# Kernel optimization log

Hardware: AMD Instinct MI355X
Metric: run time of the kernel (lower is better)

The kernel has to match this reference:

```python
import jax, jax.numpy as jnp
import numpy as np

B, D, H = 4096, 256, 1024
TRACE_STEPS = 10
T_FINAL = 1.0


def setup_inputs() -> dict:
    key = jax.random.key(0)
    k0, k1, k2 = jax.random.split(key, 3)
    s1 = 1.0 / np.sqrt(D + 1)
    s2 = 1.0 / np.sqrt(H)
    return {
        "x": jax.random.normal(k0, (B, D), dtype=jnp.float32),
        "W1": jax.random.uniform(k1, (D + 1, H), jnp.float32, -s1, s1),
        "b1": jnp.zeros((H,), jnp.float32),
        "W2": jax.random.uniform(k2, (H, D), jnp.float32, -s2, s2),
        "b2": jnp.zeros((D,), jnp.float32),
    }


def _odefun(params, t, z):
    # FFJORD vector field: tanh MLP on [z, t]. z: [B, D] -> [B, D]
    W1, b1, W2, b2 = params
    tcol = jnp.full((z.shape[0], 1), t, dtype=z.dtype)
    h = jnp.tanh(jnp.concatenate([z, tcol], axis=-1) @ W1 + b1)
    return h @ W2 + b2


def _rademacher(key, shape, dtype):
    # randint(0,2)*2-1, matching the torch probe construction
    return jax.random.randint(key, shape, 0, 2).astype(dtype) * 2.0 - 1.0


def _aug_dynamics(params, t, state, e):
    # state: [B, D+1] = [z | logp]; e: [TRACE_STEPS, B, D] Rademacher probes.
    # torch computes etf = grad((f*e).sum(), z) = e^T J, div = (e^T J)*e summed.
    # e^T J e == e . (J e), so forward-mode jvp gives identical math.
    z = state[:, :-1]
    f = lambda zz: _odefun(params, t, zz)

    def probe(ei):
        f_z, Je = jax.jvp(f, (z,), (ei,))
        return f_z, jnp.sum(Je * ei, axis=-1)  # [B]

    f_z, divs = jax.vmap(probe)(e)
    f_z = f_z[0]                       # primal identical across probes
    div_est = jnp.mean(divs, axis=0)   # average of trace_steps estimates
    return jnp.concatenate([f_z, -div_est[:, None]], axis=-1)


def reference(x, W1, b1, W2, b2):
    params = (W1, b1, W2, b2)
    Bx = x.shape[0]
    ekey = jax.random.key(42)
    probes = lambda i: _rademacher(jax.random.fold_in(ekey, i), (TRACE_STEPS, Bx, D), x.dtype)

    # initial augmented state: [z, logp=0]
    y0 = jnp.concatenate([x, jnp.zeros((Bx, 1), x.dtype)], axis=-1)

    # t_grid = [0, T] with 2 points -> fixed-grid rk4 takes ONE RK4 step of size T
    h = T_FINAL
    g = lambda t, y, i: _aug_dynamics(params, t, y, probes(i))
    k1 = g(0.0, y0, 0)
    k2 = g(0.5 * h, y0 + 0.5 * h * k1, 1)
    k3 = g(0.5 * h, y0 + 0.5 * h * k2, 2)
    k4 = g(h, y0 + h * k3, 3)
    y1 = y0 + (h / 6.0) * (k1 + 2.0 * k2 + 2.0 * k3 + k4)

    # module returns the full trajectory `output`: [len(t_grid), B, D+1]
    return jnp.stack([y0, y1], axis=0)
```

## Files before the change

kernel.cpp:

```cpp
#include <hip/hip_runtime.h>
#include <stdint.h>

#define BATCH 4096
#define DIMD  256
#define DIMH  1024
#define EPAD  264
#define NEPW  163840

typedef __attribute__((ext_vector_type(8))) short short8;
typedef __attribute__((ext_vector_type(4))) float float4v;

struct Keys4 { uint32_t a[4]; uint32_t b[4]; };

__host__ __device__ static inline uint32_t rotl32(uint32_t v, int r) {
#ifdef __HIP_DEVICE_COMPILE__
    return __builtin_amdgcn_alignbit(v, v, 32 - r);
#else
    return (v << r) | (v >> (32 - r));
#endif
}

__host__ __device__ static inline void tf2x32(uint32_t k0, uint32_t k1,
                                              uint32_t c0, uint32_t c1,
                                              uint32_t& o0, uint32_t& o1) {
    uint32_t ks0 = k0, ks1 = k1, ks2 = k0 ^ k1 ^ 0x1BD11BDAu;
    uint32_t x0 = c0 + ks0, x1 = c1 + ks1;
#define TF_R4(a, b, c, d)                                   \
    x0 += x1; x1 = rotl32(x1, a); x1 ^= x0;                 \
    x0 += x1; x1 = rotl32(x1, b); x1 ^= x0;                 \
    x0 += x1; x1 = rotl32(x1, c); x1 ^= x0;                 \
    x0 += x1; x1 = rotl32(x1, d); x1 ^= x0;
    TF_R4(13, 15, 26, 6)  x0 += ks1; x1 += ks2 + 1u;
    TF_R4(17, 29, 16, 24) x0 += ks2; x1 += ks0 + 2u;
    TF_R4(13, 15, 26, 6)  x0 += ks0; x1 += ks1 + 3u;
    TF_R4(17, 29, 16, 24) x0 += ks1; x1 += ks2 + 4u;
    TF_R4(13, 15, 26, 6)  x0 += ks2; x1 += ks0 + 5u;
#undef TF_R4
    o0 = x0; o1 = x1;
}

__device__ static inline short f2bf(float f) {
    uint32_t u = __float_as_uint(f);
    uint32_t r = (u + 0x7FFFu + ((u >> 16) & 1u)) >> 16;
    return (short)r;
}

__global__ __launch_bounds__(256) void k_prep(
    const float* __restrict__ x,  const float* __restrict__ W1,
    const float* __restrict__ W2, short* __restrict__ W1T,
    short* __restrict__ W2B, short* __restrict__ W2T,
    short* __restrict__ zb, float* __restrict__ dv,
    uint64_t* __restrict__ Ep0, uint32_t ek0, uint32_t ek1)
{
    const int idx = blockIdx.x * 256 + threadIdx.x;
    if (idx < 262144) {
        const int n = idx >> 8, d = idx & 255;
        W1T[idx] = f2bf(W1[d * DIMH + n]);
    } else if (idx < 524288) {
        const int i = idx - 262144;
        W2B[i] = f2bf(W2[i]);
    } else if (idx < 786432) {
        const int i = idx - 524288;
        const int d = i >> 10, k = i & 1023;
        W2T[i] = f2bf(W2[k * DIMD + d]);
    } else if (idx < 1835008) {
        const int i = idx - 786432;
        zb[i] = f2bf(x[i]);
    } else if (idx < 1851392) {
        dv[idx - 1835008] = 0.0f;
    } else {
        const uint32_t j = (uint32_t)(idx - 1851392);
        uint32_t y0, y1;
        tf2x32(ek0, ek1, 0u, j, y0, y1);
        uint64_t mask = __ballot(((y0 ^ y1) & 1u) != 0u);
        if ((threadIdx.x & 63) == 0)
            Ep0[j >> 6] = mask;
    }
}

__global__ __launch_bounds__(256) void k_pre_div(
    const short* __restrict__ Zb, const short* __restrict__ W1T,
    const short* __restrict__ W2B, const float* __restrict__ W1,
    const float* __restrict__ b1, float tval,
    const uint64_t* __restrict__ Ep, short* __restrict__ h_bf,
    float* __restrict__ divacc,
    uint64_t* __restrict__ EpNext, uint32_t nk0, uint32_t nk1, int do_egen)
{
    __shared__ short E[64 * EPAD];
    const int t = threadIdx.x;
    const int nt = blockIdx.x;
    const int b0 = blockIdx.y * 64;
    const int wave = t >> 6, lane = t & 63;
    const int col = lane & 15, kq = lane >> 4;
    const int n = nt * 64 + wave * 16 + col;

    short8 bufr[8];
#pragma unroll
    for (int ks = 0; ks < 8; ++ks)
        bufr[ks] = *(const short8*)&W1T[n * DIMD + ks * 32 + kq * 8];

    float sreg[4][4];
    const float add = tval * W1[DIMD * DIMH + n] + b1[n];
#pragma unroll
    for (int ms = 0; ms < 4; ++ms) {
        float4v acc = {0.f, 0.f, 0.f, 0.f};
#pragma unroll
        for (int ks = 0; ks < 8; ++ks) {
            short8 af = *(const short8*)&Zb[(b0 + ms * 16 + col) * DIMD + ks * 32 + kq * 8];
            acc = __builtin_amdgcn_mfma_f32_16x16x32_bf16(af, bufr[ks], acc, 0, 0, 0);
        }
#pragma unroll
        for (int r = 0; r < 4; ++r) {
            float hv = tanhf(acc[r] + add);
            h_bf[(b0 + ms * 16 + kq * 4 + r) * DIMH + n] = f2bf(hv);
            sreg[ms][r] = 1.0f - hv * hv;
        }
    }

    if (do_egen) {
        const uint32_t bflat = (uint32_t)(blockIdx.y * 16 + blockIdx.x);
        const uint32_t jbase = bflat * 10240u + (uint32_t)t;
#pragma unroll 2
        for (int w = 0; w < 40; ++w) {
            uint32_t j = jbase + (uint32_t)w * 256u;
            uint32_t y0, y1;
            tf2x32(nk0, nk1, 0u, j, y0, y1);
            uint64_t mask = __ballot(((y0 ^ y1) & 1u) != 0u);
            if (lane == 0)
                EpNext[j >> 6] = mask;
        }
    }

    short8 bvfr[8];
#pragma unroll
    for (int ks = 0; ks < 8; ++ks)
        bvfr[ks] = *(const short8*)&W2B[n * DIMD + ks * 32 + kq * 8];

    float rowacc[4][4];
#pragma unroll
    for (int a = 0; a < 4; ++a)
#pragma unroll
        for (int r = 0; r < 4; ++r) rowacc[a][r] = 0.0f;

    const int erow = t & 63, ecg = t >> 6;
    short* const edst = &E[erow * EPAD + ecg * 64];
    const uint64_t* const esrc = Ep + (size_t)b0 * 4 + erow * 4 + ecg;

#pragma unroll 1
    for (int probe = 0; probe < 10; ++probe) {
        __syncthreads();
        uint64_t w = esrc[(size_t)probe * BATCH * 4];
#pragma unroll
        for (int i = 0; i < 8; ++i) {
            short8 val;
#pragma unroll
            for (int k = 0; k < 8; ++k)
                val[k] = ((w >> (i * 8 + k)) & 1ull) ? (short)0x3F80 : (short)0xBF80u;
            *(short8*)&edst[i * 8] = val;
        }
        __syncthreads();

#pragma unroll
        for (int ms = 0; ms < 4; ++ms) {
            const short* arow = &E[(ms * 16 + col) * EPAD + kq * 8];
            float4v u = {0.f, 0.f, 0.f, 0.f}, v = {0.f, 0.f, 0.f, 0.f};
#pragma unroll
            for (int ks = 0; ks < 8; ++ks) {
                short8 af = *(const short8*)&arow[ks * 32];
                u = __builtin_amdgcn_mfma_f32_16x16x32_bf16(af, bufr[ks], u, 0, 0, 0);
                v = __builtin_amdgcn_mfma_f32_16x16x32_bf16(af, bvfr[ks], v, 0, 0, 0);
            }
#pragma unroll
            for (int r = 0; r < 4; ++r)
                rowacc[ms][r] += u[r] * sreg[ms][r] * v[r];
        }
    }

#pragma unroll
    for (int ms = 0; ms < 4; ++ms) {
#pragma unroll
        for (int r = 0; r < 4; ++r) {
            float p = rowacc[ms][r];
            p += __shfl_xor(p, 1, 64);
            p += __shfl_xor(p, 2, 64);
            p += __shfl_xor(p, 4, 64);
            p += __shfl_xor(p, 8, 64);
            rowacc[ms][r] = p;
        }
    }
    if (col == 0) {
#pragma unroll
        for (int ms = 0; ms < 4; ++ms)
#pragma unroll
            for (int r = 0; r < 4; ++r)
                atomicAdd(&divacc[b0 + ms * 16 + kq * 4 + r], rowacc[ms][r] * 0.1f);
    }
}

__global__ __launch_bounds__(256) void k_fz2(
    const short* __restrict__ Hb, const short* __restrict__ W2T,
    const float* __restrict__ b2, const float* __restrict__ x,
    float* __restrict__ fz, float cnext, int write_zb, short* __restrict__ zb)
{
    const int t = threadIdx.x;
    const int wave = t >> 6, lane = t & 63;
    const int col = lane & 15, kq = lane >> 4;
    const int m0 = blockIdx.x * 16;
    const int n0 = wave * 64;

    float4v acc[4];
#pragma unroll
    for (int ns = 0; ns < 4; ++ns) acc[ns] = (float4v){0.f, 0.f, 0.f, 0.f};

    const short* ap = &Hb[(m0 + col) * DIMH + kq * 8];
    short8 a_cur = *(const short8*)ap;
    short8 b_cur[4];
#pragma unroll
    for (int ns = 0; ns < 4; ++ns)
        b_cur[ns] = *(const short8*)&W2T[(n0 + ns * 16 + col) * DIMH + kq * 8];

    for (int ks = 0; ks < 31; ++ks) {
        short8 a_nxt = *(const short8*)&ap[(ks + 1) * 32];
        short8 b_nxt[4];
#pragma unroll
        for (int ns = 0; ns < 4; ++ns)
            b_nxt[ns] = *(const short8*)&W2T[(n0 + ns * 16 + col) * DIMH + (ks + 1) * 32 + kq * 8];
#pragma unroll
        for (int ns = 0; ns < 4; ++ns)
            acc[ns] = __builtin_amdgcn_mfma_f32_16x16x32_bf16(a_cur, b_cur[ns], acc[ns], 0, 0, 0);
        a_cur = a_nxt;
#pragma unroll
        for (int ns = 0; ns < 4; ++ns) b_cur[ns] = b_nxt[ns];
    }
#pragma unroll
    for (int ns = 0; ns < 4; ++ns)
        acc[ns] = __builtin_amdgcn_mfma_f32_16x16x32_bf16(a_cur, b_cur[ns], acc[ns], 0, 0, 0);

#pragma unroll
    for (int ns = 0; ns < 4; ++ns) {
        const int n = n0 + ns * 16 + col;
        const float bias = b2[n];
#pragma unroll
        for (int r = 0; r < 4; ++r) {
            const int m = m0 + kq * 4 + r;
            const float val = acc[ns][r] + bias;
            fz[m * DIMD + n] = val;
            if (write_zb)
                zb[m * DIMD + n] = f2bf(x[m * DIMD + n] + cnext * val);
        }
    }
}

__global__ __launch_bounds__(256) void k_out(
    const float* __restrict__ x, const float* __restrict__ fz,
    const float* __restrict__ divacc, float* __restrict__ out)
{
    const int idx = blockIdx.x * 256 + threadIdx.x;
    const int TOT = BATCH * (DIMD + 1);
    if (idx >= TOT) return;
    const int b = idx / (DIMD + 1);
    const int c = idx - b * (DIMD + 1);
    const float sixth = 1.0f / 6.0f;
    if (c < DIMD) {
        float xv = x[b * DIMD + c];
        int o = b * DIMD + c;
        float f1 = fz[o];
        float f2 = fz[BATCH * DIMD + o];
        float f3 = fz[2 * BATCH * DIMD + o];
        float f4 = fz[3 * BATCH * DIMD + o];
        out[idx] = xv;
        out[TOT + idx] = xv + (f1 + 2.0f * f2 + 2.0f * f3 + f4) * sixth;
    } else {
        float d1 = divacc[b];
        float d2 = divacc[BATCH + b];
        float d3 = divacc[2 * BATCH + b];
        float d4 = divacc[3 * BATCH + b];
        out[idx] = 0.0f;
        out[TOT + idx] = -(d1 + 2.0f * d2 + 2.0f * d3 + d4) * sixth;
    }
}

extern "C" void kernel_launch(void* const* d_in, const int* in_sizes, int n_in,
                              void* d_out, int out_size, void* d_ws, size_t ws_size,
                              hipStream_t stream) {
    const float* x  = (const float*)d_in[0];
    const float* W1 = (const float*)d_in[1];
    const float* b1 = (const float*)d_in[2];
    const float* W2 = (const float*)d_in[3];
    const float* b2 = (const float*)d_in[4];
    float* out = (float*)d_out;

    char* ws = (char*)d_ws;
    short* hb    = (short*)(ws);
    float* fz    = (float*)(ws + 8388608);
    short* zb    = (short*)(ws + 25165824);
    short* w1t   = (short*)(ws + 27262976);
    short* w2b   = (short*)(ws + 27787264);
    short* w2t   = (short*)(ws + 28311552);
    float* dv    = (float*)(ws + 28835840);
    uint64_t* ep = (uint64_t*)(ws + 28901376);

    Keys4 keys;
    for (uint32_t i = 0; i < 4; ++i) {
        uint32_t f0, f1, g0, g1;
        tf2x32(0u, 42u, 0u, i, f0, f1);
        tf2x32(f0, f1, 0u, 1u, g0, g1);
        keys.a[i] = g0;
        keys.b[i] = g1;
    }

    k_prep<<<48192, 256, 0, stream>>>(x, W1, W2, w1t, w2b, w2t, zb, dv,
                                      ep, keys.a[0], keys.b[0]);

    const float tvals[4] = {0.0f, 0.5f, 0.5f, 1.0f};
    const float cnext[4] = {0.5f, 0.5f, 1.0f, 0.0f};
    for (int s = 0; s < 4; ++s) {
        const int last = (s == 3);
        k_pre_div<<<dim3(16, 64), 256, 0, stream>>>(
            zb, w1t, w2b, W1, b1, tvals[s], ep + (size_t)s * NEPW,
            hb, dv + (size_t)s * BATCH,
            ep + (size_t)(s + 1) * NEPW,
            last ? 0u : keys.a[s + 1], last ? 0u : keys.b[s + 1],
            last ? 0 : 1);
        k_fz2<<<256, 256, 0, stream>>>(hb, w2t, b2, x,
                                       fz + (size_t)s * BATCH * DIMD,
                                       cnext[s], (s < 3) ? 1 : 0, zb);
    }
    int tot = BATCH * (DIMD + 1);
    k_out<<<(tot + 255) / 256, 256, 0, stream>>>(x, fz, dv, out);
}
```

Baseline: 531.9 us.

## Store probes as expanded bf16 in global memory, drop LDS staging, accumulate RK sum

Probe vectors are now written to global memory as full bf16 ±1 values (double-buffered across stages) instead of packed bitmasks. The MFMA A-operands are then read directly from global memory, which removes the LDS expansion step and the two barriers per probe. Generation of the next stage's probes is interleaved inside the probe loop. The per-stage f outputs are folded into a single running RK4 weighted sum, which shrinks the workspace and the final kernel's reads. In exchange, probe traffic grows roughly 16x (about 20 MB per stage, written and read), and uncoalesced global A-loads replace LDS reads.

Result: slower. 1.055 ms (+98.4%).

```diff
diff --git a/kernel.cpp b/kernel.cpp
--- a/kernel.cpp
+++ b/kernel.cpp
@@ -4,8 +4,7 @@
 #define BATCH 4096
 #define DIMD  256
 #define DIMH  1024
-#define EPAD  264
-#define NEPW  163840
+#define NEEL  10485760
 
 typedef __attribute__((ext_vector_type(8))) short short8;
 typedef __attribute__((ext_vector_type(4))) float float4v;
@@ -50,7 +49,7 @@
     const float* __restrict__ W2, short* __restrict__ W1T,
     short* __restrict__ W2B, short* __restrict__ W2T,
     short* __restrict__ zb, float* __restrict__ dv,
-    uint64_t* __restrict__ Ep0, uint32_t ek0, uint32_t ek1)
+    short* __restrict__ E0, uint32_t ek0, uint32_t ek1)
 {
     const int idx = blockIdx.x * 256 + threadIdx.x;
     if (idx < 262144) {
@@ -72,9 +71,7 @@
         const uint32_t j = (uint32_t)(idx - 1851392);
         uint32_t y0, y1;
         tf2x32(ek0, ek1, 0u, j, y0, y1);
-        uint64_t mask = __ballot(((y0 ^ y1) & 1u) != 0u);
-        if ((threadIdx.x & 63) == 0)
-            Ep0[j >> 6] = mask;
+        E0[j] = ((y0 ^ y1) & 1u) ? (short)0x3F80 : (short)0xBF80u;
     }
 }
 
@@ -82,11 +79,10 @@
     const short* __restrict__ Zb, const short* __restrict__ W1T,
     const short* __restrict__ W2B, const float* __restrict__ W1,
     const float* __restrict__ b1, float tval,
-    const uint64_t* __restrict__ Ep, short* __restrict__ h_bf,
+    const short* __restrict__ Ecur, short* __restrict__ h_bf,
     float* __restrict__ divacc,
-    uint64_t* __restrict__ EpNext, uint32_t nk0, uint32_t nk1, int do_egen)
+    short* __restrict__ Enext, uint32_t nk0, uint32_t nk1, int do_egen)
 {
-    __shared__ short E[64 * EPAD];
     const int t = threadIdx.x;
     const int nt = blockIdx.x;
     const int b0 = blockIdx.y * 64;
@@ -94,10 +90,12 @@
     const int col = lane & 15, kq = lane >> 4;
     const int n = nt * 64 + wave * 16 + col;
 
-    short8 bufr[8];
-#pragma unroll
-    for (int ks = 0; ks < 8; ++ks)
+    short8 bufr[8], bvfr[8];
+#pragma unroll
+    for (int ks = 0; ks < 8; ++ks) {
         bufr[ks] = *(const short8*)&W1T[n * DIMD + ks * 32 + kq * 8];
+        bvfr[ks] = *(const short8*)&W2B[n * DIMD + ks * 32 + kq * 8];
+    }
 
     float sreg[4][4];
     const float add = tval * W1[DIMD * DIMH + n] + b1[n];
@@ -117,52 +115,27 @@
         }
     }
 
-    if (do_egen) {
-        const uint32_t bflat = (uint32_t)(blockIdx.y * 16 + blockIdx.x);
-        const uint32_t jbase = bflat * 10240u + (uint32_t)t;
-#pragma unroll 2
-        for (int w = 0; w < 40; ++w) {
-            uint32_t j = jbase + (uint32_t)w * 256u;
-            uint32_t y0, y1;
-            tf2x32(nk0, nk1, 0u, j, y0, y1);
-            uint64_t mask = __ballot(((y0 ^ y1) & 1u) != 0u);
-            if (lane == 0)
-                EpNext[j >> 6] = mask;
-        }
-    }
-
-    short8 bvfr[8];
-#pragma unroll
-    for (int ks = 0; ks < 8; ++ks)
-        bvfr[ks] = *(const short8*)&W2B[n * DIMD + ks * 32 + kq * 8];
-
     float rowacc[4][4];
 #pragma unroll
     for (int a = 0; a < 4; ++a)
 #pragma unroll
         for (int r = 0; r < 4; ++r) rowacc[a][r] = 0.0f;
 
-    const int erow = t & 63, ecg = t >> 6;
-    short* const edst = &E[erow * EPAD + ecg * 64];
-    const uint64_t* const esrc = Ep + (size_t)b0 * 4 + erow * 4 + ecg;
+    const uint32_t bflat = (uint32_t)(blockIdx.y * 16 + blockIdx.x);
+    const uint32_t jbase = bflat * 10240u + (uint32_t)t;
 
 #pragma unroll 1
     for (int probe = 0; probe < 10; ++probe) {
-        __syncthreads();
-        uint64_t w = esrc[(size_t)probe * BATCH * 4];
-#pragma unroll
-        for (int i = 0; i < 8; ++i) {
-            short8 val;
-#pragma unroll
-            for (int k = 0; k < 8; ++k)
-                val[k] = ((w >> (i * 8 + k)) & 1ull) ? (short)0x3F80 : (short)0xBF80u;
-            *(short8*)&edst[i * 8] = val;
-        }
-        __syncthreads();
-
+        const short* Ep = Ecur + (size_t)probe * (BATCH * DIMD) + (size_t)b0 * DIMD;
 #pragma unroll
         for (int ms = 0; ms < 4; ++ms) {
-            const short* arow = &E[(ms * 16 + col) * EPAD + kq * 8];
+            if (do_egen) {
+                uint32_t j = jbase + (uint32_t)(probe * 4 + ms) * 256u;
+                uint32_t y0, y1;
+                tf2x32(nk0, nk1, 0u, j, y0, y1);
+                Enext[j] = ((y0 ^ y1) & 1u) ? (short)0x3F80 : (short)0xBF80u;
+            }
+            const short* arow = Ep + (ms * 16 + col) * DIMD + kq * 8;
             float4v u = {0.f, 0.f, 0.f, 0.f}, v = {0.f, 0.f, 0.f, 0.f};
 #pragma unroll
             for (int ks = 0; ks < 8; ++ks) {
@@ -200,7 +173,8 @@
 __global__ __launch_bounds__(256) void k_fz2(
     const short* __restrict__ Hb, const short* __restrict__ W2T,
     const float* __restrict__ b2, const float* __restrict__ x,
-    float* __restrict__ fz, float cnext, int write_zb, short* __restrict__ zb)
+    float* __restrict__ rksum, float cw, int first,
+    float cnext, int write_zb, short* __restrict__ zb)
 {
     const int t = threadIdx.x;
     const int wave = t >> 6, lane = t & 63;
@@ -243,16 +217,18 @@
 #pragma unroll
         for (int r = 0; r < 4; ++r) {
             const int m = m0 + kq * 4 + r;
+            const int o = m * DIMD + n;
             const float val = acc[ns][r] + bias;
-            fz[m * DIMD + n] = val;
+            const float contrib = cw * val;
+            rksum[o] = first ? contrib : (rksum[o] + contrib);
             if (write_zb)
-                zb[m * DIMD + n] = f2bf(x[m * DIMD + n] + cnext * val);
+                zb[o] = f2bf(x[o] + cnext * val);
         }
     }
 }
 
 __global__ __launch_bounds__(256) void k_out(
-    const float* __restrict__ x, const float* __restrict__ fz,
+    const float* __restrict__ x, const float* __restrict__ rksum,
     const float* __restrict__ divacc, float* __restrict__ out)
 {
     const int idx = blockIdx.x * 256 + threadIdx.x;
@@ -263,13 +239,8 @@
     const float sixth = 1.0f / 6.0f;
     if (c < DIMD) {
         float xv = x[b * DIMD + c];
-        int o = b * DIMD + c;
-        float f1 = fz[o];
-        float f2 = fz[BATCH * DIMD + o];
-        float f3 = fz[2 * BATCH * DIMD + o];
-        float f4 = fz[3 * BATCH * DIMD + o];
         out[idx] = xv;
-        out[TOT + idx] = xv + (f1 + 2.0f * f2 + 2.0f * f3 + f4) * sixth;
+        out[TOT + idx] = xv + rksum[b * DIMD + c] * sixth;
     } else {
         float d1 = divacc[b];
         float d2 = divacc[BATCH + b];
@@ -292,13 +263,14 @@
 
     char* ws = (char*)d_ws;
     short* hb    = (short*)(ws);
-    float* fz    = (float*)(ws + 8388608);
-    short* zb    = (short*)(ws + 25165824);
-    short* w1t   = (short*)(ws + 27262976);
-    short* w2b   = (short*)(ws + 27787264);
-    short* w2t   = (short*)(ws + 28311552);
-    float* dv    = (float*)(ws + 28835840);
-    uint64_t* ep = (uint64_t*)(ws + 28901376);
+    float* rksum = (float*)(ws + 8388608);
+    short* zb    = (short*)(ws + 12582912);
+    short* w1t   = (short*)(ws + 14680064);
+    short* w2b   = (short*)(ws + 15204352);
+    short* w2t   = (short*)(ws + 15728640);
+    float* dv    = (float*)(ws + 16252928);
+    short* e0    = (short*)(ws + 16318464);
+    short* e1    = (short*)(ws + 37289984);
 
     Keys4 keys;
     for (uint32_t i = 0; i < 4; ++i) {
@@ -310,22 +282,24 @@
     }
 
     k_prep<<<48192, 256, 0, stream>>>(x, W1, W2, w1t, w2b, w2t, zb, dv,
-                                      ep, keys.a[0], keys.b[0]);
+                                      e0, keys.a[0], keys.b[0]);
 
     const float tvals[4] = {0.0f, 0.5f, 0.5f, 1.0f};
     const float cnext[4] = {0.5f, 0.5f, 1.0f, 0.0f};
+    const float cw[4]    = {1.0f, 2.0f, 2.0f, 1.0f};
     for (int s = 0; s < 4; ++s) {
         const int last = (s == 3);
+        short* ecur = (s & 1) ? e1 : e0;
+        short* enxt = (s & 1) ? e0 : e1;
         k_pre_div<<<dim3(16, 64), 256, 0, stream>>>(
-            zb, w1t, w2b, W1, b1, tvals[s], ep + (size_t)s * NEPW,
+            zb, w1t, w2b, W1, b1, tvals[s], ecur,
             hb, dv + (size_t)s * BATCH,
-            ep + (size_t)(s + 1) * NEPW,
-            last ? 0u : keys.a[s + 1], last ? 0u : keys.b[s + 1],
+            enxt, last ? 0u : keys.a[s + 1], last ? 0u : keys.b[s + 1],
             last ? 0 : 1);
-        k_fz2<<<256, 256, 0, stream>>>(hb, w2t, b2, x,
-                                       fz + (size_t)s * BATCH * DIMD,
+        k_fz2<<<256, 256, 0, stream>>>(hb, w2t, b2, x, rksum,
+                                       cw[s], (s == 0) ? 1 : 0,
                                        cnext[s], (s < 3) ? 1 : 0, zb);
     }
     int tot = BATCH * (DIMD + 1);
-    k_out<<<(tot + 255) / 256, 256, 0, stream>>>(x, fz, dv, out);
-}
+    k_out<<<(tot + 255) / 256, 256, 0, stream>>>(x, rksum, dv, out);
+}
```
